# Performance work log

Hardware: AMD Instinct MI355X
Metric: run time of the kernel (lower is better)

The kernel has to match this reference:

```python
import jax, jax.numpy as jnp
import numpy as np

B, C, H, W = 4, 256, 64, 64
HALF = C // 2
BN_EPS = 1e-5


def setup_inputs() -> dict:
    key = jax.random.key(0)
    ks = jax.random.split(key, 6)
    scale = 1.0 / np.sqrt(C)
    return {
        "x": jax.random.normal(ks[0], (B, C, H, W), dtype=jnp.float32),
        "w1": jax.random.normal(ks[1], (HALF, C), dtype=jnp.float32) * scale,
        "w2": jax.random.normal(ks[2], (HALF, C), dtype=jnp.float32) * scale,
        "w3": jax.random.normal(ks[3], (HALF, C), dtype=jnp.float32) * scale,
        "w4": jax.random.normal(ks[4], (C, HALF), dtype=jnp.float32) * (1.0 / np.sqrt(HALF)),
        "gamma": jnp.ones((C,), dtype=jnp.float32),
        "beta": jnp.zeros((C,), dtype=jnp.float32),
        "running_mean": jnp.zeros((C,), dtype=jnp.float32),
        "running_var": jnp.ones((C,), dtype=jnp.float32),
    }


def _conv1x1(x, w):
    # x: [b,c,h,w], w: [out,in] -> [b,out,h,w]
    return jnp.einsum('bchw,oc->bohw', x, w)


def reference(x, w1, w2, w3, w4, gamma, beta, running_mean, running_var):
    b, Cin, h, w = x.shape
    c = Cin // 2
    hw = h * w
    n1 = _conv1x1(x, w1)  # [b,c,h,w]
    n2 = _conv1x1(x, w2)
    n3 = _conv1x1(x, w3)
    # Faithful to torch .view (raw reshape, NOT a transpose)
    q = n1.reshape(b, hw, c)   # [b,hw,c]
    k = n2.reshape(b, c, hw)   # [b,c,hw]
    attn = jnp.einsum('bic,bcj->bij', q, k)        # [b,hw,hw]
    attn = jax.nn.softmax(attn, axis=-1)
    v = n3.reshape(b, hw, c)
    res = jnp.einsum('bij,bjc->bic', attn, v)      # [b,hw,c]
    res = res.reshape(b, c, h, w)
    out = _conv1x1(res, w4)                        # [b,C,h,w]
    # BatchNorm2d in eval mode with running stats
    inv = jax.lax.rsqrt(running_var + BN_EPS)
    out = (out - running_mean[None, :, None, None]) * (gamma * inv)[None, :, None, None] + beta[None, :, None, None]
    return out + x
```

## Files before the change

### kernel.cpp

```cpp
#include <hip/hip_runtime.h>
#include <cstdint>

#define BN 4
#define CIN 256
#define HALFC 128
#define HW 4096
#define SPLIT 4
#define JT 64
#define JITERS (HW / SPLIT / JT)

typedef float  floatx4 __attribute__((ext_vector_type(4)));
typedef short  shortx8 __attribute__((ext_vector_type(8)));

#if __has_builtin(__builtin_amdgcn_exp2f)
#define EXP2F(x) __builtin_amdgcn_exp2f(x)
#else
#define EXP2F(x) exp2f(x)
#endif
#define L2E 1.44269504088896f

__device__ __forceinline__ unsigned short f2bf(float f) {
  unsigned u = __float_as_uint(f);
  u += 0x7FFFu + ((u >> 16) & 1u);
  return (unsigned short)(u >> 16);
}

__device__ __forceinline__ void async16(const void* g, void* l) {
  __builtin_amdgcn_global_load_lds((const __attribute__((address_space(1))) void*)g,
                                   (__attribute__((address_space(3))) void*)l, 16, 0, 0);
}

__global__ __launch_bounds__(256) void k_split(const float* __restrict__ x,
    const float* __restrict__ w1, const float* __restrict__ w2,
    const float* __restrict__ w3, unsigned short* __restrict__ Xth,
    unsigned short* __restrict__ Wh) {
  __shared__ float smf[64 * 65];
  int bid = blockIdx.x;
  int t = threadIdx.x;
  if (bid < 1024) {
    int b = bid >> 8, rem = bid & 255;
    int cit = rem >> 6, pxt = rem & 63;
    const float* src = x + (size_t)b * 1048576 + (size_t)(cit * 64) * HW + pxt * 64;
#pragma unroll
    for (int k = 0; k < 16; k++) {
      int idx = k * 256 + t;
      int r = idx >> 6, c = idx & 63;
      smf[r * 65 + c] = src[(size_t)r * HW + c];
    }
    __syncthreads();
    int prow = t >> 2, seg = t & 3;
    union { unsigned short us[16]; uint4 v[2]; } oh;
#pragma unroll
    for (int u = 0; u < 16; u++)
      oh.us[u] = f2bf(smf[(seg * 16 + u) * 65 + prow]);
    size_t dst = (size_t)b * 1048576 + (size_t)(pxt * 64 + prow) * 256 + cit * 64 + seg * 16;
    *(uint4*)(Xth + dst) = oh.v[0];
    *(uint4*)(Xth + dst + 8) = oh.v[1];
  } else {
    int bw = bid - 1024;
    int f0 = bw * 8192 + t * 32;
    const float* wsrc;
    int fo;
    if (f0 < 32768)      { wsrc = w1; fo = f0; }
    else if (f0 < 65536) { wsrc = w2; fo = f0 - 32768; }
    else                 { wsrc = w3; fo = f0 - 65536; }
    union { unsigned short us[32]; uint4 v[4]; } oh;
#pragma unroll
    for (int u = 0; u < 32; u++) oh.us[u] = f2bf(wsrc[fo + u]);
#pragma unroll
    for (int k = 0; k < 4; k++) *((uint4*)(Wh + f0) + k) = oh.v[k];
  }
}

__global__ __launch_bounds__(256) void k_projM(const unsigned short* __restrict__ Xth,
    const unsigned short* __restrict__ Wh, unsigned short* __restrict__ Q,
    unsigned short* __restrict__ Kt, unsigned short* __restrict__ n3) {
  __shared__ unsigned short XhS[4096];
  __shared__ unsigned short ES[9216];
  int bid = blockIdx.x;
  int pxt = bid & 31;
  int ct = bid >> 5;
  int b = ct / 6, cot = ct % 6;
  int px0 = pxt * 128, co0 = cot * 64;
  int t = threadIdx.x;
  int w = t >> 6, lane = t & 63, l16 = lane & 15, quad = lane >> 4;

  int myco = co0 + w * 16 + l16;
  shortx8 whf[8];
#pragma unroll
  for (int s = 0; s < 8; s++)
    whf[s] = *(const shortx8*)(Wh + (size_t)myco * 256 + s * 32 + quad * 8);
  floatx4 acc[8];
  floatx4 zf = {0.f, 0.f, 0.f, 0.f};
#pragma unroll
  for (int mt = 0; mt < 8; mt++) acc[mt] = zf;
  const unsigned short* XhB = Xth + (size_t)b * 1048576;
  int k8 = lane >> 4, pxm = lane & 15;

#pragma unroll
  for (int s = 0; s < 8; s++) {
    __syncthreads();
#pragma unroll
    for (int c2 = 0; c2 < 2; c2++) {
      int px = px0 + (c2 * 4 + w) * 16 + pxm;
      async16(XhB + (size_t)px * 256 + s * 32 + k8 * 8, (char*)XhS + c2 * 4096 + w * 1024);
    }
    __syncthreads();
#pragma unroll
    for (int mt = 0; mt < 8; mt++) {
      shortx8 ah = *(const shortx8*)((const char*)XhS + mt * 1024 + lane * 16);
      acc[mt] = __builtin_amdgcn_mfma_f32_16x16x32_bf16(ah, whf[s], acc[mt], 0, 0, 0);
    }
  }
  __syncthreads();
  if (cot < 2 || cot >= 4) {
    int co_l = w * 16 + l16;
#pragma unroll
    for (int mt = 0; mt < 8; mt++) {
      int px = mt * 16 + quad * 4;
      unsigned lo = (unsigned)f2bf(acc[mt][0]) | ((unsigned)f2bf(acc[mt][1]) << 16);
      unsigned hi = (unsigned)f2bf(acc[mt][2]) | ((unsigned)f2bf(acc[mt][3]) << 16);
      *(uint2*)(ES + co_l * 136 + px) = make_uint2(lo, hi);
    }
    __syncthreads();
    int cr = t >> 2, seg = t & 3;
    unsigned short* dstb = (cot < 2)
        ? Q  + (size_t)b * 524288 + (size_t)(co0 + cr) * HW
        : n3 + (size_t)b * 524288 + (size_t)(co0 - 256 + cr) * HW;
#pragma unroll
    for (int k2 = 0; k2 < 4; k2++) {
      uint4 v = *(const uint4*)(ES + cr * 136 + seg * 32 + k2 * 8);
      *(uint4*)(dstb + px0 + seg * 32 + k2 * 8) = v;
    }
  } else {
#pragma unroll
    for (int mt = 0; mt < 8; mt++)
#pragma unroll
      for (int rr = 0; rr < 4; rr++) {
        int px = mt * 16 + quad * 4 + rr;
        ES[px * 72 + w * 16 + l16] = f2bf(acc[mt][rr]);
      }
    __syncthreads();
    int ch0 = co0 - 128;
#pragma unroll
    for (int it = 0; it < 4; it++) {
      int cid = it * 256 + t;
      int px = cid >> 3, c8 = cid & 7;
      uint4 v = *(const uint4*)(ES + px * 72 + c8 * 8);
      *(uint4*)(Kt + (size_t)b * 524288 + (size_t)(px0 + px) * 128 + ch0 + c8 * 8) = v;
    }
  }
}

__global__ __launch_bounds__(256) void k_layoutVF(const unsigned short* __restrict__ n3,
    unsigned short* __restrict__ VtF) {
  __shared__ unsigned short sm[8192];
  int bid = blockIdx.x;
  int b = bid >> 6, jt = bid & 63;
  int t = threadIdx.x;
  const unsigned short* src = n3 + (size_t)b * 524288 + (size_t)(jt * 2) * 4096;
#pragma unroll
  for (int k = 0; k < 32; k++) sm[k * 256 + t] = src[k * 256 + t];
  __syncthreads();
  unsigned short* dst = VtF + (size_t)b * 524288 + (size_t)jt * 8192;
#pragma unroll
  for (int k = 0; k < 4; k++) {
    int s = k * 256 + t;
    int nt = s >> 7, kt = (s >> 6) & 1, quad = (s >> 4) & 3, l16 = s & 15;
    union { unsigned short us[8]; uint4 v; } o;
#pragma unroll
    for (int e = 0; e < 8; e++)
      o.us[e] = sm[kt * 4096 + (quad * 8 + e) * 128 + nt * 16 + l16];
    *(uint4*)(dst + s * 8) = o.v;
  }
}

__global__ __launch_bounds__(256, 2) void k_flash(const unsigned short* __restrict__ Q,
    const unsigned short* __restrict__ Kt, const unsigned short* __restrict__ VtF,
    float* __restrict__ Opart, float* __restrict__ ml) {
  __shared__ unsigned short KtS[2 * 8192];
  __shared__ unsigned short PS[4 * 32 * 64];
  int bid = blockIdx.x;
  int itile = bid & 31, sp = (bid >> 5) & 3, b = bid >> 7;
  int t = threadIdx.x;
  int w = t >> 6, lane = t & 63, l16 = lane & 15, quad = lane >> 4;
  int i0 = itile * 128;

  shortx8 qf[2][4];
#pragma unroll
  for (int ig = 0; ig < 2; ig++) {
    const unsigned short* qp = Q + ((size_t)b * HW + i0 + w * 32 + ig * 16 + l16) * 128 + quad * 8;
#pragma unroll
    for (int ks = 0; ks < 4; ks++) qf[ig][ks] = *(const shortx8*)(qp + ks * 32);
  }
  __asm__ __volatile__("s_waitcnt vmcnt(0)" ::: "memory");

  floatx4 O[2][8];
  floatx4 zf = {0.f, 0.f, 0.f, 0.f};
#pragma unroll
  for (int ig = 0; ig < 2; ig++)
#pragma unroll
    for (int nt = 0; nt < 8; nt++) O[ig][nt] = zf;
  float m_i[2] = {-1e30f, -1e30f}, l_i[2] = {0.f, 0.f};

  int ccK = w * 4 + (lane >> 4);
  const unsigned short* kbase = Kt + (size_t)b * HW * 128
                              + (size_t)(sp * 1024 + l16) * 128 + ccK * 8;
  const unsigned short* vB = VtF + (size_t)b * 524288 + (size_t)(sp * 16) * 8192 + lane * 8;
  char* Pw = (char*)PS + w * 4096;

#pragma unroll
  for (int c4 = 0; c4 < 4; c4++)
    async16(kbase + c4 * 2048, (char*)KtS + c4 * 4096 + w * 1024);

  for (int it = 0; it < JITERS; it++) {
    int cur = it & 1, nxt = cur ^ 1;
    __asm__ __volatile__("s_barrier" ::: "memory");
    shortx8 vf[8][2];
    {
      const unsigned short* vt = vB + (size_t)it * 8192;
#pragma unroll
      for (int nt = 0; nt < 8; nt++)
#pragma unroll
        for (int kt = 0; kt < 2; kt++)
          vf[nt][kt] = *(const shortx8*)(vt + (nt * 2 + kt) * 512);
    }
    if (it + 1 < JITERS) {
      const unsigned short* kp = kbase + (size_t)(it + 1) * 8192;
#pragma unroll
      for (int c4 = 0; c4 < 4; c4++)
        async16(kp + c4 * 2048, (char*)KtS + nxt * 16384 + c4 * 4096 + w * 1024);
      __asm__ __volatile__("s_waitcnt vmcnt(20)" ::: "memory");
    } else {
      __asm__ __volatile__("s_waitcnt vmcnt(16)" ::: "memory");
    }
    __asm__ __volatile__("s_barrier" ::: "memory");

    const char* kc = (const char*)KtS + cur * 16384;

    floatx4 S[2][4];
#pragma unroll
    for (int ig = 0; ig < 2; ig++)
#pragma unroll
      for (int mt = 0; mt < 4; mt++) S[ig][mt] = zf;
#pragma unroll
    for (int mt = 0; mt < 4; mt++) {
#pragma unroll
      for (int ks = 0; ks < 4; ks++) {
        shortx8 af = *(const shortx8*)(kc + mt * 4096 + ks * 1024 + lane * 16);
        S[0][mt] = __builtin_amdgcn_mfma_f32_16x16x32_bf16(af, qf[0][ks], S[0][mt], 0, 0, 0);
        S[1][mt] = __builtin_amdgcn_mfma_f32_16x16x32_bf16(af, qf[1][ks], S[1][mt], 0, 0, 0);
      }
    }
    float alpha[2];
#pragma unroll
    for (int ig = 0; ig < 2; ig++) {
      float tmax = S[ig][0][0];
#pragma unroll
      for (int mt = 0; mt < 4; mt++)
#pragma unroll
        for (int rr = 0; rr < 4; rr++) tmax = fmaxf(tmax, S[ig][mt][rr]);
      tmax = fmaxf(tmax, __shfl_xor(tmax, 16));
      tmax = fmaxf(tmax, __shfl_xor(tmax, 32));
      float mnew = fmaxf(m_i[ig], tmax);
      alpha[ig] = EXP2F((m_i[ig] - mnew) * L2E);
      float tsum = 0.f;
#pragma unroll
      for (int mt = 0; mt < 4; mt++)
#pragma unroll
        for (int rr = 0; rr < 4; rr++) {
          float p = EXP2F((S[ig][mt][rr] - mnew) * L2E);
          S[ig][mt][rr] = p;
          tsum += p;
        }
      tsum += __shfl_xor(tsum, 16);
      tsum += __shfl_xor(tsum, 32);
      l_i[ig] = l_i[ig] * alpha[ig] + tsum;
      m_i[ig] = mnew;
    }
    if (__ballot(alpha[0] < 1.f || alpha[1] < 1.f)) {
#pragma unroll
      for (int ig = 0; ig < 2; ig++) {
        float ar[4];
#pragma unroll
        for (int rr = 0; rr < 4; rr++) ar[rr] = __shfl(alpha[ig], quad * 4 + rr);
#pragma unroll
        for (int nt = 0; nt < 8; nt++)
#pragma unroll
          for (int rr = 0; rr < 4; rr++) O[ig][nt][rr] *= ar[rr];
      }
    }
#pragma unroll
    for (int ig = 0; ig < 2; ig++)
#pragma unroll
      for (int mt = 0; mt < 4; mt++) {
        unsigned lo = __builtin_amdgcn_perm(__float_as_uint(S[ig][mt][1]),
                                            __float_as_uint(S[ig][mt][0]), 0x07060302u);
        unsigned hi = __builtin_amdgcn_perm(__float_as_uint(S[ig][mt][3]),
                                            __float_as_uint(S[ig][mt][2]), 0x07060302u);
        *(uint2*)(Pw + ig * 2048 + (mt * 2 + (quad >> 1)) * 256 + l16 * 16 + (quad & 1) * 8)
            = make_uint2(lo, hi);
      }
    __asm__ __volatile__("s_waitcnt lgkmcnt(0)" ::: "memory");
    if (it + 1 < JITERS) {
      __asm__ __volatile__("s_waitcnt vmcnt(4)" ::: "memory");
    } else {
      __asm__ __volatile__("s_waitcnt vmcnt(0)" ::: "memory");
    }
#pragma unroll
    for (int kt = 0; kt < 2; kt++) {
      shortx8 pf0 = *(const shortx8*)(Pw + kt * 1024 + lane * 16);
      shortx8 pf1 = *(const shortx8*)(Pw + 2048 + kt * 1024 + lane * 16);
#pragma unroll
      for (int nt = 0; nt < 8; nt++) {
        O[0][nt] = __builtin_amdgcn_mfma_f32_16x16x32_bf16(pf0, vf[nt][kt], O[0][nt], 0, 0, 0);
        O[1][nt] = __builtin_amdgcn_mfma_f32_16x16x32_bf16(pf1, vf[nt][kt], O[1][nt], 0, 0, 0);
      }
    }
  }
#pragma unroll
  for (int ig = 0; ig < 2; ig++) {
    float* Ob = Opart + ((size_t)(sp * 4 + b) * HW + i0 + w * 32 + ig * 16) * 128;
#pragma unroll
    for (int nt = 0; nt < 8; nt++)
#pragma unroll
      for (int rr = 0; rr < 4; rr++)
        Ob[(size_t)(quad * 4 + rr) * 128 + nt * 16 + l16] = O[ig][nt][rr];
  }
  if (quad == 0) {
    float2* mlp = (float2*)ml;
#pragma unroll
    for (int ig = 0; ig < 2; ig++)
      mlp[(size_t)(sp * 4 + b) * HW + i0 + w * 32 + ig * 16 + l16]
          = make_float2(m_i[ig], l_i[ig]);
  }
}

__global__ __launch_bounds__(256) void k_merge(const float* __restrict__ Opart,
    const float* __restrict__ ml, float* __restrict__ res) {
  size_t e = (size_t)blockIdx.x * 256 + threadIdx.x;
  int cq = (int)(e & 31);
  int i = (int)((e >> 5) & 4095);
  int b = (int)(e >> 17);
  const float2* mlp = (const float2*)ml;
  float m[SPLIT], l[SPLIT];
  float M = -1e30f;
#pragma unroll
  for (int s = 0; s < SPLIT; s++) {
    float2 st = mlp[(size_t)(s * 4 + b) * HW + i];
    m[s] = st.x; l[s] = st.y;
    M = fmaxf(M, m[s]);
  }
  float denom = 0.f;
  float wgt[SPLIT];
#pragma unroll
  for (int s = 0; s < SPLIT; s++) {
    float ws_ = EXP2F((m[s] - M) * L2E);
    wgt[s] = ws_;
    denom += l[s] * ws_;
  }
  float inv = 1.f / denom;
  floatx4 acc = {0.f, 0.f, 0.f, 0.f};
#pragma unroll
  for (int s = 0; s < SPLIT; s++) {
    floatx4 v = *(const floatx4*)(Opart + ((size_t)(s * 4 + b) * HW + i) * 128 + cq * 4);
    acc += v * (wgt[s] * inv);
  }
  *(floatx4*)(res + e * 4) = acc;
}

__global__ __launch_bounds__(256) void k_out(const float* __restrict__ res,
    const float* __restrict__ w4, const float* __restrict__ gamma,
    const float* __restrict__ beta, const float* __restrict__ rmean,
    const float* __restrict__ rvar, const float* __restrict__ x,
    float* __restrict__ out) {
  __shared__ float wt[16 * 128];
  int bid = blockIdx.x;
  int cot = bid & 15;
  int st = (bid >> 4) & 15;
  int b = bid >> 8;
  int t = threadIdx.x;
  int co0 = cot * 16;
#pragma unroll
  for (int k = 0; k < 8; k++) wt[k * 256 + t] = w4[(size_t)co0 * 128 + k * 256 + t];
  __syncthreads();
  int px = st * 256 + t;
  const float* rb = res + (size_t)b * 524288 + px;
  float acc[16];
#pragma unroll
  for (int r = 0; r < 16; r++) acc[r] = 0.f;
  for (int ci = 0; ci < 128; ci += 4) {
    float xv[4];
#pragma unroll
    for (int kk = 0; kk < 4; kk++) xv[kk] = rb[(size_t)(ci + kk) * HW];
#pragma unroll
    for (int r = 0; r < 16; r++) {
      floatx4 wv = *(const floatx4*)&wt[r * 128 + ci];
#pragma unroll
      for (int kk = 0; kk < 4; kk++) acc[r] += wv[kk] * xv[kk];
    }
  }
  const float* xb = x + ((size_t)b * 256 + co0) * HW + px;
  float* ob = out + ((size_t)b * 256 + co0) * HW + px;
#pragma unroll
  for (int r = 0; r < 16; r++) {
    int co = co0 + r;
    float g = gamma[co] * rsqrtf(rvar[co] + 1e-5f);
    float bb = beta[co] - rmean[co] * g;
    ob[(size_t)r * HW] = acc[r] * g + bb + xb[(size_t)r * HW];
  }
}

extern "C" void kernel_launch(void* const* d_in, const int* in_sizes, int n_in,
                              void* d_out, int out_size, void* d_ws, size_t ws_size,
                              hipStream_t stream) {
  const float* x     = (const float*)d_in[0];
  const float* w1    = (const float*)d_in[1];
  const float* w2    = (const float*)d_in[2];
  const float* w3    = (const float*)d_in[3];
  const float* w4    = (const float*)d_in[4];
  const float* gamma = (const float*)d_in[5];
  const float* beta  = (const float*)d_in[6];
  const float* rmean = (const float*)d_in[7];
  const float* rvar  = (const float*)d_in[8];
  float* out = (float*)d_out;
  char* ws = (char*)d_ws;

  size_t off = (size_t)SPLIT * 4 * HW * 128 * 4;
  float* Opart = (float*)ws;
  unsigned short* n3  = (unsigned short*)ws;
  unsigned short* Xth = (unsigned short*)(ws + ((size_t)8 << 20));
  unsigned short* Q   = (unsigned short*)(ws + off); off += (size_t)4 * HW * 128 * 2;
  unsigned short* Kt  = (unsigned short*)(ws + off); off += (size_t)4 * HW * 128 * 2;
  unsigned short* VtF = (unsigned short*)(ws + off); off += (size_t)4 * HW * 128 * 2;
  float* ml  = (float*)(ws + off); off += (size_t)SPLIT * 4 * HW * 2 * 4;
  float* res = (float*)(ws + off); off += (size_t)4 * HW * 128 * 4;
  unsigned short* Wh = (unsigned short*)(ws + off); off += (size_t)384 * 256 * 2;
  if (ws_size < off) return;

  k_split   <<<1036, 256, 0, stream>>>(x, w1, w2, w3, Xth, Wh);
  k_projM   <<<768,  256, 0, stream>>>(Xth, Wh, Q, Kt, n3);
  k_layoutVF<<<256,  256, 0, stream>>>(n3, VtF);
  k_flash   <<<512,  256, 0, stream>>>(Q, Kt, VtF, Opart, ml);
  k_merge   <<<2048, 256, 0, stream>>>(Opart, ml, res);
  k_out     <<<1024, 256, 0, stream>>>(res, w4, gamma, beta, rmean, rvar, x, out);
}
```

Before: 190.3 us.

## Retune flash attention: lazy rescale, 6-way KV split, split V loads, setprio

The flash kernel is templated on the KV split count. It uses 6 splits (768 blocks, launch bounds 3) when the workspace is large enough, and a block-index swizzle spreads the work. The online softmax now rescales only when the tile max exceeds the running max by more than 8, which skips the alpha exp and O rescale on most iterations. V fragments are loaded in two halves so fewer registers are live, and s_setprio is raised around the MFMA bursts. The goal is better occupancy and less softmax overhead, at the cost of a larger merge, uneven split lengths, and some exp values that can exceed 1 before normalisation.

```diff
diff --git a/kernel.cpp b/kernel.cpp
--- a/kernel.cpp
+++ b/kernel.cpp
@@ -5,9 +5,6 @@
 #define CIN 256
 #define HALFC 128
 #define HW 4096
-#define SPLIT 4
-#define JT 64
-#define JITERS (HW / SPLIT / JT)
 
 typedef float  floatx4 __attribute__((ext_vector_type(4)));
 typedef short  shortx8 __attribute__((ext_vector_type(8)));
@@ -175,13 +172,21 @@
   }
 }
 
-__global__ __launch_bounds__(256, 2) void k_flash(const unsigned short* __restrict__ Q,
+template<int NSP>
+__global__ __launch_bounds__(256, 3) void k_flash(const unsigned short* __restrict__ Q,
     const unsigned short* __restrict__ Kt, const unsigned short* __restrict__ VtF,
     float* __restrict__ Opart, float* __restrict__ ml) {
   __shared__ unsigned short KtS[2 * 8192];
   __shared__ unsigned short PS[4 * 32 * 64];
-  int bid = blockIdx.x;
-  int itile = bid & 31, sp = (bid >> 5) & 3, b = bid >> 7;
+  constexpr int nb = 128 * NSP;
+  constexpr int jq = 64 / NSP, jr = 64 % NSP;
+  int bid0 = blockIdx.x;
+  int bid = (bid0 & 7) * (nb >> 3) + (bid0 >> 3);
+  int itile = bid & 31;
+  int g = bid >> 5;
+  int sp = g % NSP, b = g / NSP;
+  int jiters = jq + (sp < jr ? 1 : 0);
+  int jt0 = sp * jq + (sp < jr ? sp : jr);
   int t = threadIdx.x;
   int w = t >> 6, lane = t & 63, l16 = lane & 15, quad = lane >> 4;
   int i0 = itile * 128;
@@ -203,36 +208,35 @@
     for (int nt = 0; nt < 8; nt++) O[ig][nt] = zf;
   float m_i[2] = {-1e30f, -1e30f}, l_i[2] = {0.f, 0.f};
 
-  int ccK = w * 4 + (lane >> 4);
+  int ccK = w * 4 + quad;
   const unsigned short* kbase = Kt + (size_t)b * HW * 128
-                              + (size_t)(sp * 1024 + l16) * 128 + ccK * 8;
-  const unsigned short* vB = VtF + (size_t)b * 524288 + (size_t)(sp * 16) * 8192 + lane * 8;
+                              + (size_t)(jt0 * 64 + l16) * 128 + ccK * 8;
+  const unsigned short* vB = VtF + (size_t)b * 524288 + (size_t)jt0 * 8192 + lane * 8;
   char* Pw = (char*)PS + w * 4096;
 
 #pragma unroll
   for (int c4 = 0; c4 < 4; c4++)
     async16(kbase + c4 * 2048, (char*)KtS + c4 * 4096 + w * 1024);
 
-  for (int it = 0; it < JITERS; it++) {
+  for (int it = 0; it < jiters; it++) {
     int cur = it & 1, nxt = cur ^ 1;
     __asm__ __volatile__("s_barrier" ::: "memory");
-    shortx8 vf[8][2];
-    {
-      const unsigned short* vt = vB + (size_t)it * 8192;
-#pragma unroll
-      for (int nt = 0; nt < 8; nt++)
-#pragma unroll
-        for (int kt = 0; kt < 2; kt++)
-          vf[nt][kt] = *(const shortx8*)(vt + (nt * 2 + kt) * 512);
-    }
-    if (it + 1 < JITERS) {
+    shortx8 vf0[4][2];
+    const unsigned short* vt = vB + (size_t)it * 8192;
+#pragma unroll
+    for (int nt = 0; nt < 4; nt++)
+#pragma unroll
+      for (int kt = 0; kt < 2; kt++)
+        vf0[nt][kt] = *(const shortx8*)(vt + (nt * 2 + kt) * 512);
+    bool hasn = (it + 1 < jiters);
+    if (hasn) {
       const unsigned short* kp = kbase + (size_t)(it + 1) * 8192;
 #pragma unroll
       for (int c4 = 0; c4 < 4; c4++)
         async16(kp + c4 * 2048, (char*)KtS + nxt * 16384 + c4 * 4096 + w * 1024);
-      __asm__ __volatile__("s_waitcnt vmcnt(20)" ::: "memory");
+      __asm__ __volatile__("s_waitcnt vmcnt(12)" ::: "memory");
     } else {
-      __asm__ __volatile__("s_waitcnt vmcnt(16)" ::: "memory");
+      __asm__ __volatile__("s_waitcnt vmcnt(8)" ::: "memory");
     }
     __asm__ __volatile__("s_barrier" ::: "memory");
 
@@ -243,6 +247,7 @@
     for (int ig = 0; ig < 2; ig++)
 #pragma unroll
       for (int mt = 0; mt < 4; mt++) S[ig][mt] = zf;
+    __builtin_amdgcn_s_setprio(1);
 #pragma unroll
     for (int mt = 0; mt < 4; mt++) {
 #pragma unroll
@@ -252,35 +257,27 @@
         S[1][mt] = __builtin_amdgcn_mfma_f32_16x16x32_bf16(af, qf[1][ks], S[1][mt], 0, 0, 0);
       }
     }
-    float alpha[2];
+    __builtin_amdgcn_s_setprio(0);
+
+    float tmax[2];
 #pragma unroll
     for (int ig = 0; ig < 2; ig++) {
-      float tmax = S[ig][0][0];
-#pragma unroll
-      for (int mt = 0; mt < 4; mt++)
-#pragma unroll
-        for (int rr = 0; rr < 4; rr++) tmax = fmaxf(tmax, S[ig][mt][rr]);
-      tmax = fmaxf(tmax, __shfl_xor(tmax, 16));
-      tmax = fmaxf(tmax, __shfl_xor(tmax, 32));
-      float mnew = fmaxf(m_i[ig], tmax);
-      alpha[ig] = EXP2F((m_i[ig] - mnew) * L2E);
-      float tsum = 0.f;
-#pragma unroll
-      for (int mt = 0; mt < 4; mt++)
-#pragma unroll
-        for (int rr = 0; rr < 4; rr++) {
-          float p = EXP2F((S[ig][mt][rr] - mnew) * L2E);
-          S[ig][mt][rr] = p;
-          tsum += p;
-        }
-      tsum += __shfl_xor(tsum, 16);
-      tsum += __shfl_xor(tsum, 32);
-      l_i[ig] = l_i[ig] * alpha[ig] + tsum;
-      m_i[ig] = mnew;
-    }
-    if (__ballot(alpha[0] < 1.f || alpha[1] < 1.f)) {
+      float a0 = fmaxf(fmaxf(S[ig][0][0], S[ig][0][1]), fmaxf(S[ig][0][2], S[ig][0][3]));
+      float a1 = fmaxf(fmaxf(S[ig][1][0], S[ig][1][1]), fmaxf(S[ig][1][2], S[ig][1][3]));
+      float a2 = fmaxf(fmaxf(S[ig][2][0], S[ig][2][1]), fmaxf(S[ig][2][2], S[ig][2][3]));
+      float a3 = fmaxf(fmaxf(S[ig][3][0], S[ig][3][1]), fmaxf(S[ig][3][2], S[ig][3][3]));
+      float tm = fmaxf(fmaxf(a0, a1), fmaxf(a2, a3));
+      tm = fmaxf(tm, __shfl_xor(tm, 16));
+      tm = fmaxf(tm, __shfl_xor(tm, 32));
+      tmax[ig] = tm;
+    }
+    float alpha[2] = {1.f, 1.f};
+    if (__ballot(tmax[0] > m_i[0] + 8.f || tmax[1] > m_i[1] + 8.f)) {
 #pragma unroll
       for (int ig = 0; ig < 2; ig++) {
+        float mn = fmaxf(m_i[ig], tmax[ig]);
+        alpha[ig] = EXP2F((m_i[ig] - mn) * L2E);
+        m_i[ig] = mn;
         float ar[4];
 #pragma unroll
         for (int rr = 0; rr < 4; rr++) ar[rr] = __shfl(alpha[ig], quad * 4 + rr);
@@ -291,7 +288,22 @@
       }
     }
 #pragma unroll
-    for (int ig = 0; ig < 2; ig++)
+    for (int ig = 0; ig < 2; ig++) {
+      float nsc = m_i[ig] * L2E;
+      float sm[4];
+#pragma unroll
+      for (int mt = 0; mt < 4; mt++) {
+        float p0 = EXP2F(fmaf(S[ig][mt][0], L2E, -nsc));
+        float p1 = EXP2F(fmaf(S[ig][mt][1], L2E, -nsc));
+        float p2 = EXP2F(fmaf(S[ig][mt][2], L2E, -nsc));
+        float p3 = EXP2F(fmaf(S[ig][mt][3], L2E, -nsc));
+        S[ig][mt][0] = p0; S[ig][mt][1] = p1; S[ig][mt][2] = p2; S[ig][mt][3] = p3;
+        sm[mt] = (p0 + p1) + (p2 + p3);
+      }
+      float ts = (sm[0] + sm[1]) + (sm[2] + sm[3]);
+      ts += __shfl_xor(ts, 16);
+      ts += __shfl_xor(ts, 32);
+      l_i[ig] = l_i[ig] * alpha[ig] + ts;
 #pragma unroll
       for (int mt = 0; mt < 4; mt++) {
         unsigned lo = __builtin_amdgcn_perm(__float_as_uint(S[ig][mt][1]),
@@ -301,22 +313,44 @@
         *(uint2*)(Pw + ig * 2048 + (mt * 2 + (quad >> 1)) * 256 + l16 * 16 + (quad & 1) * 8)
             = make_uint2(lo, hi);
       }
+    }
+    shortx8 vf1[4][2];
+#pragma unroll
+    for (int nt = 0; nt < 4; nt++)
+#pragma unroll
+      for (int kt = 0; kt < 2; kt++)
+        vf1[nt][kt] = *(const shortx8*)(vt + ((nt + 4) * 2 + kt) * 512);
     __asm__ __volatile__("s_waitcnt lgkmcnt(0)" ::: "memory");
-    if (it + 1 < JITERS) {
-      __asm__ __volatile__("s_waitcnt vmcnt(4)" ::: "memory");
+    if (hasn) {
+      __asm__ __volatile__("s_waitcnt vmcnt(12)" ::: "memory");
     } else {
-      __asm__ __volatile__("s_waitcnt vmcnt(0)" ::: "memory");
-    }
+      __asm__ __volatile__("s_waitcnt vmcnt(8)" ::: "memory");
+    }
+    __builtin_amdgcn_s_setprio(1);
 #pragma unroll
     for (int kt = 0; kt < 2; kt++) {
       shortx8 pf0 = *(const shortx8*)(Pw + kt * 1024 + lane * 16);
       shortx8 pf1 = *(const shortx8*)(Pw + 2048 + kt * 1024 + lane * 16);
 #pragma unroll
-      for (int nt = 0; nt < 8; nt++) {
-        O[0][nt] = __builtin_amdgcn_mfma_f32_16x16x32_bf16(pf0, vf[nt][kt], O[0][nt], 0, 0, 0);
-        O[1][nt] = __builtin_amdgcn_mfma_f32_16x16x32_bf16(pf1, vf[nt][kt], O[1][nt], 0, 0, 0);
-      }
-    }
+      for (int nt = 0; nt < 4; nt++) {
+        O[0][nt] = __builtin_amdgcn_mfma_f32_16x16x32_bf16(pf0, vf0[nt][kt], O[0][nt], 0, 0, 0);
+        O[1][nt] = __builtin_amdgcn_mfma_f32_16x16x32_bf16(pf1, vf0[nt][kt], O[1][nt], 0, 0, 0);
+      }
+    }
+    __builtin_amdgcn_s_setprio(0);
+    __asm__ __volatile__("s_waitcnt vmcnt(0)" ::: "memory");
+    __builtin_amdgcn_s_setprio(1);
+#pragma unroll
+    for (int kt = 0; kt < 2; kt++) {
+      shortx8 pf0 = *(const shortx8*)(Pw + kt * 1024 + lane * 16);
+      shortx8 pf1 = *(const shortx8*)(Pw + 2048 + kt * 1024 + lane * 16);
+#pragma unroll
+      for (int nt = 0; nt < 4; nt++) {
+        O[0][nt + 4] = __builtin_amdgcn_mfma_f32_16x16x32_bf16(pf0, vf1[nt][kt], O[0][nt + 4], 0, 0, 0);
+        O[1][nt + 4] = __builtin_amdgcn_mfma_f32_16x16x32_bf16(pf1, vf1[nt][kt], O[1][nt + 4], 0, 0, 0);
+      }
+    }
+    __builtin_amdgcn_s_setprio(0);
   }
 #pragma unroll
   for (int ig = 0; ig < 2; ig++) {
@@ -336,6 +370,7 @@
   }
 }
 
+template<int NSP>
 __global__ __launch_bounds__(256) void k_merge(const float* __restrict__ Opart,
     const float* __restrict__ ml, float* __restrict__ res) {
   size_t e = (size_t)blockIdx.x * 256 + threadIdx.x;
@@ -343,18 +378,18 @@
   int i = (int)((e >> 5) & 4095);
   int b = (int)(e >> 17);
   const float2* mlp = (const float2*)ml;
-  float m[SPLIT], l[SPLIT];
+  float m[NSP], l[NSP];
   float M = -1e30f;
 #pragma unroll
-  for (int s = 0; s < SPLIT; s++) {
+  for (int s = 0; s < NSP; s++) {
     float2 st = mlp[(size_t)(s * 4 + b) * HW + i];
     m[s] = st.x; l[s] = st.y;
     M = fmaxf(M, m[s]);
   }
   float denom = 0.f;
-  float wgt[SPLIT];
-#pragma unroll
-  for (int s = 0; s < SPLIT; s++) {
+  float wgt[NSP];
+#pragma unroll
+  for (int s = 0; s < NSP; s++) {
     float ws_ = EXP2F((m[s] - M) * L2E);
     wgt[s] = ws_;
     denom += l[s] * ws_;
@@ -362,7 +397,7 @@
   float inv = 1.f / denom;
   floatx4 acc = {0.f, 0.f, 0.f, 0.f};
 #pragma unroll
-  for (int s = 0; s < SPLIT; s++) {
+  for (int s = 0; s < NSP; s++) {
     floatx4 v = *(const floatx4*)(Opart + ((size_t)(s * 4 + b) * HW + i) * 128 + cq * 4);
     acc += v * (wgt[s] * inv);
   }
@@ -409,6 +444,15 @@
     float bb = beta[co] - rmean[co] * g;
     ob[(size_t)r * HW] = acc[r] * g + bb + xb[(size_t)r * HW];
   }
+}
+
+static size_t ws_need(int nsp) {
+  size_t off = (size_t)nsp * 4 * HW * 128 * 4;
+  off += (size_t)4 * HW * 128 * 2 * 3;
+  off += (size_t)nsp * 4 * HW * 2 * 4;
+  off += (size_t)4 * HW * 128 * 4;
+  off += (size_t)384 * 256 * 2;
+  return off;
 }
 
 extern "C" void kernel_launch(void* const* d_in, const int* in_sizes, int n_in,
@@ -426,22 +470,29 @@
   float* out = (float*)d_out;
   char* ws = (char*)d_ws;
 
-  size_t off = (size_t)SPLIT * 4 * HW * 128 * 4;
+  const int nsp = (ws_size >= ws_need(6)) ? 6 : 4;
+  if (ws_size < ws_need(4)) return;
+
+  size_t off = (size_t)nsp * 4 * HW * 128 * 4;
   float* Opart = (float*)ws;
   unsigned short* n3  = (unsigned short*)ws;
   unsigned short* Xth = (unsigned short*)(ws + ((size_t)8 << 20));
   unsigned short* Q   = (unsigned short*)(ws + off); off += (size_t)4 * HW * 128 * 2;
   unsigned short* Kt  = (unsigned short*)(ws + off); off += (size_t)4 * HW * 128 * 2;
   unsigned short* VtF = (unsigned short*)(ws + off); off += (size_t)4 * HW * 128 * 2;
-  float* ml  = (float*)(ws + off); off += (size_t)SPLIT * 4 * HW * 2 * 4;
+  float* ml  = (float*)(ws + off); off += (size_t)nsp * 4 * HW * 2 * 4;
   float* res = (float*)(ws + off); off += (size_t)4 * HW * 128 * 4;
   unsigned short* Wh = (unsigned short*)(ws + off); off += (size_t)384 * 256 * 2;
-  if (ws_size < off) return;
 
   k_split   <<<1036, 256, 0, stream>>>(x, w1, w2, w3, Xth, Wh);
   k_projM   <<<768,  256, 0, stream>>>(Xth, Wh, Q, Kt, n3);
   k_layoutVF<<<256,  256, 0, stream>>>(n3, VtF);
-  k_flash   <<<512,  256, 0, stream>>>(Q, Kt, VtF, Opart, ml);
-  k_merge   <<<2048, 256, 0, stream>>>(Opart, ml, res);
+  if (nsp == 6) {
+    k_flash<6><<<768,  256, 0, stream>>>(Q, Kt, VtF, Opart, ml);
+    k_merge<6><<<2048, 256, 0, stream>>>(Opart, ml, res);
+  } else {
+    k_flash<4><<<512,  256, 0, stream>>>(Q, Kt, VtF, Opart, ml);
+    k_merge<4><<<2048, 256, 0, stream>>>(Opart, ml, res);
+  }
   k_out     <<<1024, 256, 0, stream>>>(res, w4, gamma, beta, rmean, rvar, x, out);
 }
```

Result: slower. 248.3 us (+30.4%).

## Add lazy softmax rescale threshold, setprio around MFMAs, and block swizzle

Applied to the files above, without the earlier changes.

Changes the online softmax so the running max and O-accumulator rescale update only when a tile's max exceeds the old max by more than 8, skipping most rescales. Exponentials become a single fma plus exp2, and the reductions are written as trees. Adds s_setprio around the MFMA loops so waves in the matrix phase get issue priority over waves in softmax, and remaps block IDs so neighbouring blocks fall on different batch/split combinations. The stale max can let p reach about e^8 before rescaling, which risks bf16/fp32 range and accuracy, but the final normalisation by l stays consistent.

```diff
diff --git a/kernel.cpp b/kernel.cpp
--- a/kernel.cpp
+++ b/kernel.cpp
@@ -180,7 +180,8 @@
     float* __restrict__ Opart, float* __restrict__ ml) {
   __shared__ unsigned short KtS[2 * 8192];
   __shared__ unsigned short PS[4 * 32 * 64];
-  int bid = blockIdx.x;
+  int bid0 = blockIdx.x;
+  int bid = (bid0 & 7) * 64 + (bid0 >> 3);
   int itile = bid & 31, sp = (bid >> 5) & 3, b = bid >> 7;
   int t = threadIdx.x;
   int w = t >> 6, lane = t & 63, l16 = lane & 15, quad = lane >> 4;
@@ -203,7 +204,7 @@
     for (int nt = 0; nt < 8; nt++) O[ig][nt] = zf;
   float m_i[2] = {-1e30f, -1e30f}, l_i[2] = {0.f, 0.f};
 
-  int ccK = w * 4 + (lane >> 4);
+  int ccK = w * 4 + quad;
   const unsigned short* kbase = Kt + (size_t)b * HW * 128
                               + (size_t)(sp * 1024 + l16) * 128 + ccK * 8;
   const unsigned short* vB = VtF + (size_t)b * 524288 + (size_t)(sp * 16) * 8192 + lane * 8;
@@ -243,6 +244,7 @@
     for (int ig = 0; ig < 2; ig++)
 #pragma unroll
       for (int mt = 0; mt < 4; mt++) S[ig][mt] = zf;
+    __builtin_amdgcn_s_setprio(1);
 #pragma unroll
     for (int mt = 0; mt < 4; mt++) {
 #pragma unroll
@@ -252,35 +254,27 @@
         S[1][mt] = __builtin_amdgcn_mfma_f32_16x16x32_bf16(af, qf[1][ks], S[1][mt], 0, 0, 0);
       }
     }
-    float alpha[2];
+    __builtin_amdgcn_s_setprio(0);
+
+    float tmax[2];
 #pragma unroll
     for (int ig = 0; ig < 2; ig++) {
-      float tmax = S[ig][0][0];
-#pragma unroll
-      for (int mt = 0; mt < 4; mt++)
-#pragma unroll
-        for (int rr = 0; rr < 4; rr++) tmax = fmaxf(tmax, S[ig][mt][rr]);
-      tmax = fmaxf(tmax, __shfl_xor(tmax, 16));
-      tmax = fmaxf(tmax, __shfl_xor(tmax, 32));
-      float mnew = fmaxf(m_i[ig], tmax);
-      alpha[ig] = EXP2F((m_i[ig] - mnew) * L2E);
-      float tsum = 0.f;
-#pragma unroll
-      for (int mt = 0; mt < 4; mt++)
-#pragma unroll
-        for (int rr = 0; rr < 4; rr++) {
-          float p = EXP2F((S[ig][mt][rr] - mnew) * L2E);
-          S[ig][mt][rr] = p;
-          tsum += p;
-        }
-      tsum += __shfl_xor(tsum, 16);
-      tsum += __shfl_xor(tsum, 32);
-      l_i[ig] = l_i[ig] * alpha[ig] + tsum;
-      m_i[ig] = mnew;
-    }
-    if (__ballot(alpha[0] < 1.f || alpha[1] < 1.f)) {
+      float a0 = fmaxf(fmaxf(S[ig][0][0], S[ig][0][1]), fmaxf(S[ig][0][2], S[ig][0][3]));
+      float a1 = fmaxf(fmaxf(S[ig][1][0], S[ig][1][1]), fmaxf(S[ig][1][2], S[ig][1][3]));
+      float a2 = fmaxf(fmaxf(S[ig][2][0], S[ig][2][1]), fmaxf(S[ig][2][2], S[ig][2][3]));
+      float a3 = fmaxf(fmaxf(S[ig][3][0], S[ig][3][1]), fmaxf(S[ig][3][2], S[ig][3][3]));
+      float tm = fmaxf(fmaxf(a0, a1), fmaxf(a2, a3));
+      tm = fmaxf(tm, __shfl_xor(tm, 16));
+      tm = fmaxf(tm, __shfl_xor(tm, 32));
+      tmax[ig] = tm;
+    }
+    float alpha[2] = {1.f, 1.f};
+    if (__ballot(tmax[0] > m_i[0] + 8.f || tmax[1] > m_i[1] + 8.f)) {
 #pragma unroll
       for (int ig = 0; ig < 2; ig++) {
+        float mn = fmaxf(m_i[ig], tmax[ig]);
+        alpha[ig] = EXP2F((m_i[ig] - mn) * L2E);
+        m_i[ig] = mn;
         float ar[4];
 #pragma unroll
         for (int rr = 0; rr < 4; rr++) ar[rr] = __shfl(alpha[ig], quad * 4 + rr);
@@ -291,7 +285,22 @@
       }
     }
 #pragma unroll
-    for (int ig = 0; ig < 2; ig++)
+    for (int ig = 0; ig < 2; ig++) {
+      float nsc = m_i[ig] * L2E;
+      float sm[4];
+#pragma unroll
+      for (int mt = 0; mt < 4; mt++) {
+        float p0 = EXP2F(fmaf(S[ig][mt][0], L2E, -nsc));
+        float p1 = EXP2F(fmaf(S[ig][mt][1], L2E, -nsc));
+        float p2 = EXP2F(fmaf(S[ig][mt][2], L2E, -nsc));
+        float p3 = EXP2F(fmaf(S[ig][mt][3], L2E, -nsc));
+        S[ig][mt][0] = p0; S[ig][mt][1] = p1; S[ig][mt][2] = p2; S[ig][mt][3] = p3;
+        sm[mt] = (p0 + p1) + (p2 + p3);
+      }
+      float ts = (sm[0] + sm[1]) + (sm[2] + sm[3]);
+      ts += __shfl_xor(ts, 16);
+      ts += __shfl_xor(ts, 32);
+      l_i[ig] = l_i[ig] * alpha[ig] + ts;
 #pragma unroll
       for (int mt = 0; mt < 4; mt++) {
         unsigned lo = __builtin_amdgcn_perm(__float_as_uint(S[ig][mt][1]),
@@ -301,12 +310,14 @@
         *(uint2*)(Pw + ig * 2048 + (mt * 2 + (quad >> 1)) * 256 + l16 * 16 + (quad & 1) * 8)
             = make_uint2(lo, hi);
       }
+    }
     __asm__ __volatile__("s_waitcnt lgkmcnt(0)" ::: "memory");
     if (it + 1 < JITERS) {
       __asm__ __volatile__("s_waitcnt vmcnt(4)" ::: "memory");
     } else {
       __asm__ __volatile__("s_waitcnt vmcnt(0)" ::: "memory");
     }
+    __builtin_amdgcn_s_setprio(1);
 #pragma unroll
     for (int kt = 0; kt < 2; kt++) {
       shortx8 pf0 = *(const shortx8*)(Pw + kt * 1024 + lane * 16);
@@ -317,6 +328,7 @@
         O[1][nt] = __builtin_amdgcn_mfma_f32_16x16x32_bf16(pf1, vf[nt][kt], O[1][nt], 0, 0, 0);
       }
     }
+    __builtin_amdgcn_s_setprio(0);
   }
 #pragma unroll
   for (int ig = 0; ig < 2; ig++) {
```

New measurement: 191.2 us. About the same (+0.5%).
